# Performance work log

Measured on AMD Instinct MI355X. Metric: run time of the kernel, lower is better.

Reference implementation:

```python
import jax, jax.numpy as jnp
import numpy as np
import math

D_MODEL = 1024
NUM_HEADS = 16
HEAD_DIM = D_MODEL // NUM_HEADS
BATCH = 2
SEQ = 2048
THETA = 10000.0


def _rope_tables(seq_len, head_dim, theta=THETA):
    inv_freq = 1.0 / theta ** (jnp.arange(0, head_dim, 2, dtype=jnp.float32) / head_dim)
    pos = jnp.arange(seq_len, dtype=jnp.float32)
    freqs = jnp.outer(pos, inv_freq)                 # [S, hd/2]
    emb = jnp.concatenate([freqs, freqs], axis=-1)   # [S, hd]
    return jnp.cos(emb), jnp.sin(emb)


def _rotate_half(x):
    x1, x2 = jnp.split(x, 2, axis=-1)
    return jnp.concatenate([-x2, x1], axis=-1)


def setup_inputs() -> dict:
    key = jax.random.key(0)
    k1, k2, k3 = jax.random.split(key, 3)
    x = jax.random.normal(k1, (BATCH, SEQ, D_MODEL), dtype=jnp.float32)
    # causal mask: 1 where attend allowed, 0 where masked
    mask = jnp.tril(jnp.ones((SEQ, SEQ), dtype=jnp.int32))[None, None]
    w_qkv = jax.random.normal(k2, (D_MODEL, 3 * D_MODEL), dtype=jnp.float32) / math.sqrt(D_MODEL)
    w_out = jax.random.normal(k3, (D_MODEL, D_MODEL), dtype=jnp.float32) / math.sqrt(D_MODEL)
    return {"x": x, "mask": mask, "w_qkv": w_qkv, "w_out": w_out}


def reference(x, mask, w_qkv, w_out):
    B, S, _ = x.shape
    qkv = x @ w_qkv                                          # [B,S,3*D]
    qkv = qkv.reshape(B, S, 3, NUM_HEADS, HEAD_DIM)
    qkv = jnp.transpose(qkv, (2, 0, 3, 1, 4))                # [3,B,H,S,hd]
    q, k, v = qkv[0], qkv[1], qkv[2]
    cos, sin = _rope_tables(S, HEAD_DIM)                     # [S,hd]
    cos = cos[None, None]; sin = sin[None, None]
    q = q * cos + _rotate_half(q) * sin
    k = k * cos + _rotate_half(k) * sin
    scores = jnp.einsum('bhqd,bhkd->bhqk', q, k) / math.sqrt(HEAD_DIM)
    scores = jnp.where(mask == 0, -jnp.inf, scores)
    attn = jax.nn.softmax(scores, axis=-1)                   # dropout p=0 (eval)
    out = jnp.einsum('bhqk,bhkd->bhqd', attn, v)             # [B,H,S,hd]
    out = jnp.transpose(out, (0, 2, 1, 3)).reshape(B, S, D_MODEL)
    return out @ w_out
```

## Files before the change

### kernel.cpp

```cpp
#include <hip/hip_runtime.h>

typedef __bf16 bf16;
typedef __bf16 bf16x4 __attribute__((ext_vector_type(4)));
typedef __bf16 bf16x8 __attribute__((ext_vector_type(8)));
typedef short s16x4 __attribute__((ext_vector_type(4)));
typedef float f32x4 __attribute__((ext_vector_type(4)));

constexpr int BATCH = 2;
constexpr int SEQ   = 2048;
constexpr int DMODEL= 1024;
constexpr int NH    = 16;
constexpr int HD    = 64;
constexpr int M_ROWS= BATCH * SEQ;
constexpr int N_QKV = 3 * DMODEL;

__device__ __forceinline__ void gl_lds16(const bf16* g, bf16* l) {
  __builtin_amdgcn_global_load_lds(
      (const __attribute__((address_space(1))) unsigned int*)g,
      (__attribute__((address_space(3))) unsigned int*)l, 16, 0, 0);
}

__device__ __forceinline__ f32x4 mfma_16x16x16_bf16(bf16x4 a, bf16x4 b,
                                                    f32x4 c) {
#if defined(__HIP_DEVICE_COMPILE__)
  union { bf16x4 h; s16x4 s; } ua{a}, ub{b};
  return __builtin_amdgcn_mfma_f32_16x16x16bf16_1k(ua.s, ub.s, c, 0, 0, 0);
#else
  return c;
#endif
}

__global__ __launch_bounds__(256) void prep_kernel(
    const float* __restrict__ x, const float* __restrict__ w_qkv,
    const float* __restrict__ w_out, bf16* __restrict__ xb,
    bf16* __restrict__ WqkvT, bf16* __restrict__ WoutT) {
  const int bx = blockIdx.x, t = threadIdx.x;
  if (bx < 2048) {
    const int i = (bx * 256 + t) * 8;
    float4 f0 = *(const float4*)&x[i];
    float4 f1 = *(const float4*)&x[i + 4];
    bf16x8 v;
    v[0] = (bf16)f0.x; v[1] = (bf16)f0.y; v[2] = (bf16)f0.z; v[3] = (bf16)f0.w;
    v[4] = (bf16)f1.x; v[5] = (bf16)f1.y; v[6] = (bf16)f1.z; v[7] = (bf16)f1.w;
    *(bf16x8*)&xb[i] = v;
    return;
  }
  __shared__ float tile[32][33];
  const float* src;
  bf16* dst;
  int R, C, c0, r0;
  if (bx < 5120) {
    const int idx = bx - 2048;
    src = w_qkv; dst = WqkvT; R = DMODEL; C = N_QKV;
    c0 = (idx % 96) * 32; r0 = (idx / 96) * 32;
  } else {
    const int idx = bx - 5120;
    src = w_out; dst = WoutT; R = DMODEL; C = DMODEL;
    c0 = (idx & 31) * 32; r0 = (idx >> 5) * 32;
  }
  const int tx = t & 31, ty = t >> 5;
#pragma unroll
  for (int i = 0; i < 4; i++)
    tile[ty + 8 * i][tx] = src[(size_t)(r0 + ty + 8 * i) * C + c0 + tx];
  __syncthreads();
#pragma unroll
  for (int i = 0; i < 4; i++)
    dst[(size_t)(c0 + ty + 8 * i) * R + r0 + tx] = (bf16)tile[tx][ty + 8 * i];
}

#define GEMM_BODY(A, BT, K)                                                    \
  __shared__ bf16 smem[8448];                                                  \
  bf16* As = smem;                                                             \
  bf16* Bs = smem + 4096;                                                      \
  const int t = threadIdx.x;                                                   \
  const int m0 = blockIdx.y * 128;                                             \
  const int n0 = blockIdx.x * 128;                                             \
  const int w = t >> 6, lane = t & 63, g = lane >> 4, li = lane & 15;          \
  const int r0w = (w & 1) * 64, c0w = (w >> 1) * 64;                           \
  f32x4 acc[4][4] = {};                                                        \
  for (int k0 = 0; k0 < (K); k0 += 32) {                                       \
    __syncthreads();                                                           \
    _Pragma("unroll") for (int c = 0; c < 2; c++) {                            \
      const int idx = (w * 2 + c) * 64 + lane;                                 \
      const int row = idx >> 2, col = (idx & 3) * 8;                           \
      gl_lds16(&(A)[(size_t)(m0 + row) * (K) + k0 + col],                      \
               &As[(w * 2 + c) * 512]);                                        \
      gl_lds16(&(BT)[(size_t)(n0 + row) * (K) + k0 + col],                     \
               &Bs[(w * 2 + c) * 512]);                                        \
    }                                                                          \
    __syncthreads();                                                           \
    bf16x8 a[4], b[4];                                                         \
    _Pragma("unroll") for (int mt = 0; mt < 4; mt++)                           \
        a[mt] = *(const bf16x8*)&As[(r0w + mt * 16 + li) * 32 + g * 8];        \
    _Pragma("unroll") for (int nt = 0; nt < 4; nt++)                           \
        b[nt] = *(const bf16x8*)&Bs[(c0w + nt * 16 + li) * 32 + g * 8];        \
    _Pragma("unroll") for (int mt = 0; mt < 4; mt++)                           \
        _Pragma("unroll") for (int nt = 0; nt < 4; nt++)                       \
            acc[mt][nt] = __builtin_amdgcn_mfma_f32_16x16x32_bf16(             \
                a[mt], b[nt], acc[mt][nt], 0, 0, 0);                           \
  }

__global__ __launch_bounds__(256) void gemm_out64(
    const bf16* __restrict__ A, const bf16* __restrict__ BT,
    float* __restrict__ C, int M, int N, int K) {
  __shared__ bf16 As[64 * 32];
  __shared__ bf16 Bs[128 * 32];
  const int t = threadIdx.x;
  const int m0 = blockIdx.y * 64;
  const int n0 = blockIdx.x * 128;
  const int w = t >> 6, lane = t & 63, g = lane >> 4, li = lane & 15;
  const int r0w = (w & 1) * 32, c0w = (w >> 1) * 64;
  f32x4 acc[2][4] = {};
  for (int k0 = 0; k0 < K; k0 += 32) {
    __syncthreads();
    {
      const int idx = w * 64 + lane;
      const int row = idx >> 2, col = (idx & 3) * 8;
      gl_lds16(&A[(size_t)(m0 + row) * K + k0 + col], &As[w * 512]);
    }
#pragma unroll
    for (int c = 0; c < 2; c++) {
      const int idx = (w * 2 + c) * 64 + lane;
      const int row = idx >> 2, col = (idx & 3) * 8;
      gl_lds16(&BT[(size_t)(n0 + row) * K + k0 + col], &Bs[(w * 2 + c) * 512]);
    }
    __syncthreads();
    bf16x8 a[2], b[4];
#pragma unroll
    for (int mt = 0; mt < 2; mt++)
      a[mt] = *(const bf16x8*)&As[(r0w + mt * 16 + li) * 32 + g * 8];
#pragma unroll
    for (int nt = 0; nt < 4; nt++)
      b[nt] = *(const bf16x8*)&Bs[(c0w + nt * 16 + li) * 32 + g * 8];
#pragma unroll
    for (int mt = 0; mt < 2; mt++)
#pragma unroll
      for (int nt = 0; nt < 4; nt++)
        acc[mt][nt] = __builtin_amdgcn_mfma_f32_16x16x32_bf16(
            a[mt], b[nt], acc[mt][nt], 0, 0, 0);
  }
#pragma unroll
  for (int mt = 0; mt < 2; mt++)
#pragma unroll
    for (int nt = 0; nt < 4; nt++)
#pragma unroll
      for (int r = 0; r < 4; r++) {
        const int m = m0 + r0w + mt * 16 + g * 4 + r;
        const int n = n0 + c0w + nt * 16 + li;
        C[(size_t)m * N + n] = acc[mt][nt][r];
      }
}

__global__ __launch_bounds__(256) void gemm_qkv_rope(
    const bf16* __restrict__ A, const bf16* __restrict__ BT,
    bf16* __restrict__ Qb, bf16* __restrict__ Kb, bf16* __restrict__ Vt) {
  constexpr int K = DMODEL;
  GEMM_BODY(A, BT, K)

  const int region = n0 >> 10;
  const int b = m0 >> 11;
  const int h = ((n0 + c0w) >> 6) & 15;
  const size_t bh = (size_t)(b * NH + h);

  if (region < 2) {
    bf16* dst = region == 0 ? Qb : Kb;
    const float outsc = region == 0 ? 0.125f * 1.44269504f : 1.f;
    const float L = 13.287712379549449f;
    const float if0 = exp2f(-(float)(2 * li) / 64.f * L);
    const float if1 = exp2f(-(float)(2 * (li + 16)) / 64.f * L);
    bf16* lw = smem + w * 2112;
#pragma unroll
    for (int pass = 0; pass < 2; pass++) {
      __syncthreads();
#pragma unroll
      for (int mtl = 0; mtl < 2; mtl++) {
        const int mt = pass * 2 + mtl;
#pragma unroll
        for (int r = 0; r < 4; r++) {
          const int s = (m0 + r0w + mt * 16 + g * 4 + r) & (SEQ - 1);
          float cs[2], sn[2];
          __sincosf((float)s * if0, &sn[0], &cs[0]);
          __sincosf((float)s * if1, &sn[1], &cs[1]);
#pragma unroll
          for (int nt = 0; nt < 4; nt++) {
            const int par = nt & 1;
            const float a = acc[mt][nt][r];
            const float ap = acc[mt][nt ^ 2][r];
            const float v = (nt < 2) ? a * cs[par] - ap * sn[par]
                                     : a * cs[par] + ap * sn[par];
            lw[(mtl * 16 + g * 4 + r) * 66 + nt * 16 + li] =
                (bf16)(v * outsc);
          }
        }
      }
      __syncthreads();
      const int rowl = lane >> 1, dh = (lane & 1) * 32;
      const int s = (m0 + r0w + pass * 32 + rowl) & (SEQ - 1);
      bf16* gdst = &dst[(bh * SEQ + s) * HD + dh];
      const bf16* lsrc = &lw[rowl * 66 + dh];
#pragma unroll
      for (int c = 0; c < 4; c++)
        *(bf16x8*)&gdst[c * 8] = *(const bf16x8*)&lsrc[c * 8];
    }
  } else {
#pragma unroll
    for (int mt = 0; mt < 4; mt++)
#pragma unroll
      for (int nt = 0; nt < 4; nt++) {
        const int s = (m0 + r0w + mt * 16 + g * 4) & (SEQ - 1);
        const int d = nt * 16 + li;
        bf16x4 v;
#pragma unroll
        for (int r = 0; r < 4; r++) v[r] = (bf16)acc[mt][nt][r];
        *(bf16x4*)&Vt[(bh * HD + d) * SEQ + s] = v;
      }
  }
}

__device__ const unsigned char WORK_TAB[48] = {
    125, 126, 121, 60,
    122, 117, 118, 113, 56,
    114, 109, 110, 105, 52,
    106, 101, 102, 97,  48,
    98,  93,  94,  89,  44,
    90,  85,  86,  81,  40,
    82,  77,  78,  73,  36,
    74,  69,  70,  65,  32,
    66,  28,
    24,  20,  16,  12,  8,   4,   0};

__global__ __launch_bounds__(256, 4) void flash_attn11(
    const bf16* __restrict__ Q, const bf16* __restrict__ Kb,
    const bf16* __restrict__ Vt, bf16* __restrict__ Oout,
    float* __restrict__ Opart, float* __restrict__ Lpart) {
  const int bx = blockIdx.x;
  const int e = WORK_TAB[bx >> 5];
  const int qt = e >> 2, code = e & 3;
  const int bh = bx & 31;
  const int q0 = qt * 64;
  const int jmid = (qt + 2) >> 1;
  const int jlo = (code == 2) ? jmid : 0;
  const int jhi = (code == 1) ? jmid : qt + 1;
  const int t = threadIdx.x, w = t >> 6, lane = t & 63, g = lane >> 4,
            li = lane & 15;

  __shared__ bf16 Ks[2][4096];
  __shared__ bf16 Vs[2][4096];

  const bf16* Qh = Q  + (size_t)bh * SEQ * HD;
  const bf16* Kh = Kb + (size_t)bh * SEQ * HD;
  const bf16* Vh = Vt + (size_t)bh * HD * SEQ;

  const int qw = q0 + w * 16;

  bf16x8 qf[2];
#pragma unroll
  for (int ks = 0; ks < 2; ks++)
    qf[ks] = *(const bf16x8*)&Qh[(size_t)(qw + li) * HD + ks * 32 + g * 8];

  f32x4 o[4] = {};
  f32x4 o4  = {};
  bf16x4 ones;
#pragma unroll
  for (int r = 0; r < 4; r++) ones[r] = (bf16)1.f;

  const int p0 = w * 128 + lane, p1 = p0 + 64;
  const int sr0 = p0 >> 3, sc0 = ((p0 & 7) ^ (sr0 & 7)) * 8;
  const int sr1 = p1 >> 3, sc1 = ((p1 & 7) ^ (sr1 & 7)) * 8;
  const int lo0 = w * 1024, lo1 = w * 1024 + 512;

  {
    const int jn = jlo * 64;
    gl_lds16(&Kh[(size_t)(jn + sr0) * HD + sc0], &Ks[jlo & 1][lo0]);
    gl_lds16(&Kh[(size_t)(jn + sr1) * HD + sc1], &Ks[jlo & 1][lo1]);
    gl_lds16(&Vh[(size_t)sr0 * SEQ + jn + sc0], &Vs[jlo & 1][lo0]);
    gl_lds16(&Vh[(size_t)sr1 * SEQ + jn + sc1], &Vs[jlo & 1][lo1]);
  }
  __syncthreads();

  for (int ti = jlo; ti < jhi; ++ti) {
    const int j0 = ti * 64;
    const int cur = ti & 1, nxt = cur ^ 1;
    if (ti + 1 < jhi) {
      const int jn = j0 + 64;
      gl_lds16(&Kh[(size_t)(jn + sr0) * HD + sc0], &Ks[nxt][lo0]);
      gl_lds16(&Kh[(size_t)(jn + sr1) * HD + sc1], &Ks[nxt][lo1]);
      gl_lds16(&Vh[(size_t)sr0 * SEQ + jn + sc0], &Vs[nxt][lo0]);
      gl_lds16(&Vh[(size_t)sr1 * SEQ + jn + sc1], &Vs[nxt][lo1]);
    }

    if (j0 <= qw + 15) {
      const bool masked = (j0 + 63 > qw);
      const int ntlim = min(4, ((qw + 15 - j0) >> 4) + 1);

      f32x4 sacc[4] = {};
#pragma unroll
      for (int ks = 0; ks < 2; ks++)
#pragma unroll
        for (int nt = 0; nt < 4; nt++) {
          if (nt >= ntlim) continue;
          const int rK = nt * 16 + li;
          const int pK = rK * 8 + ((ks * 4 + g) ^ (li & 7));
          bf16x8 kf = *(const bf16x8*)&Ks[cur][pK * 8];
          sacc[nt] = __builtin_amdgcn_mfma_f32_16x16x32_bf16(kf, qf[ks],
                                                             sacc[nt], 0, 0, 0);
        }

      bf16x4 pf[4];
#pragma unroll
      for (int nt = 0; nt < 4; nt++) {
        if (nt >= ntlim) continue;
#pragma unroll
        for (int r = 0; r < 4; r++) {
          float v = sacc[nt][r];
          if (masked) {
            const int kk = j0 + nt * 16 + g * 4 + r;
            v = (kk <= qw + li) ? v : -1e30f;
          }
          pf[nt][r] = (bf16)exp2f(v);
        }
      }

#pragma unroll
      for (int nt = 0; nt < 4; nt++) {
        if (nt >= ntlim) continue;
        o4 = mfma_16x16x16_bf16(ones, pf[nt], o4);
#pragma unroll
        for (int dt = 0; dt < 4; dt++) {
          const int rV = dt * 16 + li;
          const int cg = nt * 2 + (g >> 1);
          const int pV = rV * 8 + (cg ^ (rV & 7));
          bf16x4 vfrag = *(const bf16x4*)&Vs[cur][pV * 8 + (g & 1) * 4];
          o[dt] = mfma_16x16x16_bf16(vfrag, pf[nt], o[dt]);
        }
      }
    }
    __syncthreads();
  }

  if (code == 0) {
    const float inv_l = 1.f / o4[0];
    const int b = bh >> 4, h = bh & 15;
    const int s = qw + li;
#pragma unroll
    for (int dt = 0; dt < 4; dt++) {
      bf16x4 ov;
#pragma unroll
      for (int r = 0; r < 4; r++) ov[r] = (bf16)(o[dt][r] * inv_l);
      *(bf16x4*)&Oout[((size_t)(b * SEQ + s)) * DMODEL + h * 64 + dt * 16 +
                      g * 4] = ov;
    }
  } else {
    const int srel = qw + li - 1024;
    const size_t slot = ((size_t)(bh * 2 + (code - 1)) * 1024 + srel);
    if (g == 0) Lpart[slot] = o4[0];
    float* od = &Opart[slot * 64];
#pragma unroll
    for (int dt = 0; dt < 4; dt++)
      *(f32x4*)&od[dt * 16 + g * 4] = o[dt];
  }
}

__global__ __launch_bounds__(256) void attn_merge(
    const float* __restrict__ Opart, const float* __restrict__ Lpart,
    bf16* __restrict__ attn) {
  const int gi = blockIdx.x * 256 + threadIdx.x;
  const int row = gi >> 3;
  const int d0 = (gi & 7) * 8;
  const int bh = row >> 10, srel = row & 1023;
  const int b = bh >> 4, h = bh & 15, s = srel + 1024;
  const size_t s0 = ((size_t)(bh * 2) * 1024 + srel);
  const size_t s1 = s0 + 1024;
  const float inv = 1.f / (Lpart[s0] + Lpart[s1]);
  const float* p0 = &Opart[s0 * 64 + d0];
  const float* p1 = &Opart[s1 * 64 + d0];
  float4 a0 = *(const float4*)p0;
  float4 a1 = *(const float4*)(p0 + 4);
  float4 b0 = *(const float4*)p1;
  float4 b1 = *(const float4*)(p1 + 4);
  bf16x8 v;
  v[0] = (bf16)((a0.x + b0.x) * inv); v[1] = (bf16)((a0.y + b0.y) * inv);
  v[2] = (bf16)((a0.z + b0.z) * inv); v[3] = (bf16)((a0.w + b0.w) * inv);
  v[4] = (bf16)((a1.x + b1.x) * inv); v[5] = (bf16)((a1.y + b1.y) * inv);
  v[6] = (bf16)((a1.z + b1.z) * inv); v[7] = (bf16)((a1.w + b1.w) * inv);
  *(bf16x8*)&attn[((size_t)(b * SEQ + s)) * DMODEL + h * 64 + d0] = v;
}

extern "C" void kernel_launch(void* const* d_in, const int* in_sizes, int n_in,
                              void* d_out, int out_size, void* d_ws,
                              size_t ws_size, hipStream_t stream) {
  const float* x     = (const float*)d_in[0];
  const float* w_qkv = (const float*)d_in[2];
  const float* w_out = (const float*)d_in[3];
  float* out = (float*)d_out;

  char* ws = (char*)d_ws;
  bf16* WqkvT = (bf16*)(ws);
  bf16* WoutT = (bf16*)(ws + 6291456);
  bf16* xb    = (bf16*)(ws + 8388608);
  bf16* Qb    = (bf16*)(ws + 16777216);
  bf16* Kbuf  = (bf16*)(ws + 25165824);
  bf16* Vt    = (bf16*)(ws + 33554432);
  bf16* attn  = (bf16*)(ws + 41943040);
  float* Opart= (float*)(ws + 50331648);
  float* Lpart= (float*)(ws + 67108864);

  prep_kernel<<<dim3(6144), 256, 0, stream>>>(x, w_qkv, w_out, xb, WqkvT,
                                              WoutT);
  gemm_qkv_rope<<<dim3(N_QKV / 128, M_ROWS / 128), 256, 0, stream>>>(
      xb, WqkvT, Qb, Kbuf, Vt);
  flash_attn11<<<dim3(1536), 256, 0, stream>>>(Qb, Kbuf, Vt, attn, Opart,
                                               Lpart);
  attn_merge<<<dim3(1024), 256, 0, stream>>>(Opart, Lpart, attn);
  gemm_out64<<<dim3(DMODEL / 128, M_ROWS / 64), 256, 0, stream>>>(
      attn, WoutT, out, M_ROWS, DMODEL, DMODEL);
}
```

Measured before the change: 202.6 us.

## Read K/V fragments directly from global memory instead of LDS double-buffering

The flash-attention kernel drops its double-buffered shared-memory staging of K and V tiles, the async global-to-LDS copies and the per-tile barriers. Each wave now loads its K and V MFMA fragments straight from global memory and relies on L1/L2 caching, since the four waves of a block share tiles. The block-to-(batch,head) mapping is also remapped so that eight consecutive blocks cover different heads of the same work item, changing cache locality. This removes LDS traffic and synchronisation but duplicates global loads across waves and exposes their latency without explicit prefetch.

```diff
diff --git a/kernel.cpp b/kernel.cpp
--- a/kernel.cpp
+++ b/kernel.cpp
@@ -229,14 +229,15 @@
     66,  28,
     24,  20,  16,  12,  8,   4,   0};
 
-__global__ __launch_bounds__(256, 4) void flash_attn11(
+__global__ __launch_bounds__(256, 4) void flash_attn12(
     const bf16* __restrict__ Q, const bf16* __restrict__ Kb,
     const bf16* __restrict__ Vt, bf16* __restrict__ Oout,
     float* __restrict__ Opart, float* __restrict__ Lpart) {
   const int bx = blockIdx.x;
-  const int e = WORK_TAB[bx >> 5];
+  const int j = bx >> 3;
+  const int e = WORK_TAB[j >> 2];
   const int qt = e >> 2, code = e & 3;
-  const int bh = bx & 31;
+  const int bh = (bx & 7) | ((j & 3) << 3);
   const int q0 = qt * 64;
   const int jmid = (qt + 2) >> 1;
   const int jlo = (code == 2) ? jmid : 0;
@@ -244,9 +245,6 @@
   const int t = threadIdx.x, w = t >> 6, lane = t & 63, g = lane >> 4,
             li = lane & 15;
 
-  __shared__ bf16 Ks[2][4096];
-  __shared__ bf16 Vs[2][4096];
-
   const bf16* Qh = Q  + (size_t)bh * SEQ * HD;
   const bf16* Kh = Kb + (size_t)bh * SEQ * HD;
   const bf16* Vh = Vt + (size_t)bh * HD * SEQ;
@@ -264,78 +262,50 @@
 #pragma unroll
   for (int r = 0; r < 4; r++) ones[r] = (bf16)1.f;
 
-  const int p0 = w * 128 + lane, p1 = p0 + 64;
-  const int sr0 = p0 >> 3, sc0 = ((p0 & 7) ^ (sr0 & 7)) * 8;
-  const int sr1 = p1 >> 3, sc1 = ((p1 & 7) ^ (sr1 & 7)) * 8;
-  const int lo0 = w * 1024, lo1 = w * 1024 + 512;
-
-  {
-    const int jn = jlo * 64;
-    gl_lds16(&Kh[(size_t)(jn + sr0) * HD + sc0], &Ks[jlo & 1][lo0]);
-    gl_lds16(&Kh[(size_t)(jn + sr1) * HD + sc1], &Ks[jlo & 1][lo1]);
-    gl_lds16(&Vh[(size_t)sr0 * SEQ + jn + sc0], &Vs[jlo & 1][lo0]);
-    gl_lds16(&Vh[(size_t)sr1 * SEQ + jn + sc1], &Vs[jlo & 1][lo1]);
-  }
-  __syncthreads();
-
   for (int ti = jlo; ti < jhi; ++ti) {
     const int j0 = ti * 64;
-    const int cur = ti & 1, nxt = cur ^ 1;
-    if (ti + 1 < jhi) {
-      const int jn = j0 + 64;
-      gl_lds16(&Kh[(size_t)(jn + sr0) * HD + sc0], &Ks[nxt][lo0]);
-      gl_lds16(&Kh[(size_t)(jn + sr1) * HD + sc1], &Ks[nxt][lo1]);
-      gl_lds16(&Vh[(size_t)sr0 * SEQ + jn + sc0], &Vs[nxt][lo0]);
-      gl_lds16(&Vh[(size_t)sr1 * SEQ + jn + sc1], &Vs[nxt][lo1]);
-    }
-
-    if (j0 <= qw + 15) {
-      const bool masked = (j0 + 63 > qw);
-      const int ntlim = min(4, ((qw + 15 - j0) >> 4) + 1);
-
-      f32x4 sacc[4] = {};
-#pragma unroll
-      for (int ks = 0; ks < 2; ks++)
-#pragma unroll
-        for (int nt = 0; nt < 4; nt++) {
-          if (nt >= ntlim) continue;
-          const int rK = nt * 16 + li;
-          const int pK = rK * 8 + ((ks * 4 + g) ^ (li & 7));
-          bf16x8 kf = *(const bf16x8*)&Ks[cur][pK * 8];
-          sacc[nt] = __builtin_amdgcn_mfma_f32_16x16x32_bf16(kf, qf[ks],
-                                                             sacc[nt], 0, 0, 0);
-        }
-
-      bf16x4 pf[4];
+    if (j0 > qw + 15) continue;
+    const bool masked = (j0 + 63 > qw);
+    const int ntlim = min(4, ((qw + 15 - j0) >> 4) + 1);
+
+    f32x4 sacc[4] = {};
+#pragma unroll
+    for (int ks = 0; ks < 2; ks++)
 #pragma unroll
       for (int nt = 0; nt < 4; nt++) {
         if (nt >= ntlim) continue;
-#pragma unroll
-        for (int r = 0; r < 4; r++) {
-          float v = sacc[nt][r];
-          if (masked) {
-            const int kk = j0 + nt * 16 + g * 4 + r;
-            v = (kk <= qw + li) ? v : -1e30f;
-          }
-          pf[nt][r] = (bf16)exp2f(v);
+        bf16x8 kf = *(const bf16x8*)&Kh[(size_t)(j0 + nt * 16 + li) * HD +
+                                        ks * 32 + g * 8];
+        sacc[nt] = __builtin_amdgcn_mfma_f32_16x16x32_bf16(kf, qf[ks],
+                                                           sacc[nt], 0, 0, 0);
+      }
+
+    bf16x4 pf[4];
+#pragma unroll
+    for (int nt = 0; nt < 4; nt++) {
+      if (nt >= ntlim) continue;
+#pragma unroll
+      for (int r = 0; r < 4; r++) {
+        float v = sacc[nt][r];
+        if (masked) {
+          const int kk = j0 + nt * 16 + g * 4 + r;
+          v = (kk <= qw + li) ? v : -1e30f;
         }
-      }
-
-#pragma unroll
-      for (int nt = 0; nt < 4; nt++) {
-        if (nt >= ntlim) continue;
-        o4 = mfma_16x16x16_bf16(ones, pf[nt], o4);
-#pragma unroll
-        for (int dt = 0; dt < 4; dt++) {
-          const int rV = dt * 16 + li;
-          const int cg = nt * 2 + (g >> 1);
-          const int pV = rV * 8 + (cg ^ (rV & 7));
-          bf16x4 vfrag = *(const bf16x4*)&Vs[cur][pV * 8 + (g & 1) * 4];
-          o[dt] = mfma_16x16x16_bf16(vfrag, pf[nt], o[dt]);
-        }
-      }
-    }
-    __syncthreads();
+        pf[nt][r] = (bf16)exp2f(v);
+      }
+    }
+
+#pragma unroll
+    for (int nt = 0; nt < 4; nt++) {
+      if (nt >= ntlim) continue;
+      o4 = mfma_16x16x16_bf16(ones, pf[nt], o4);
+#pragma unroll
+      for (int dt = 0; dt < 4; dt++) {
+        bf16x4 vfrag = *(const bf16x4*)&Vh[(size_t)(dt * 16 + li) * SEQ + j0 +
+                                           nt * 16 + g * 4];
+        o[dt] = mfma_16x16x16_bf16(vfrag, pf[nt], o[dt]);
+      }
+    }
   }
 
   if (code == 0) {
@@ -409,7 +379,7 @@
                                               WoutT);
   gemm_qkv_rope<<<dim3(N_QKV / 128, M_ROWS / 128), 256, 0, stream>>>(
       xb, WqkvT, Qb, Kbuf, Vt);
-  flash_attn11<<<dim3(1536), 256, 0, stream>>>(Qb, Kbuf, Vt, attn, Opart,
+  flash_attn12<<<dim3(1536), 256, 0, stream>>>(Qb, Kbuf, Vt, attn, Opart,
                                                Lpart);
   attn_merge<<<dim3(1024), 256, 0, stream>>>(Opart, Lpart, attn);
   gemm_out64<<<dim3(DMODEL / 128, M_ROWS / 64), 256, 0, stream>>>(
```

Measured after the change: 337.3 us. +66.5%, slower.
